# Performance work log

Hardware: AMD Instinct MI355X
Metric: run time of the kernel (lower is better)

The kernel has to match this reference:

```python
import jax, jax.numpy as jnp
import numpy as np
import math

D_MODEL = 1024
N_HEADS = 16
HEAD_DIM = D_MODEL // N_HEADS  # 64
SEQ_LEN = 4096
LINFORMER_K = 128
BATCH = 4


def setup_inputs() -> dict:
    key = jax.random.key(0)
    ks = jax.random.split(key, 8)
    s = 0.02  # small init so softmax is not saturated
    return {
        "x": jax.random.normal(ks[0], (BATCH, SEQ_LEN, D_MODEL), dtype=jnp.float32),
        "Wq": jax.random.normal(ks[1], (D_MODEL, D_MODEL), dtype=jnp.float32) * s,
        "bq": jnp.zeros((D_MODEL,), dtype=jnp.float32),
        "Wk": jax.random.normal(ks[2], (D_MODEL, D_MODEL), dtype=jnp.float32) * s,
        "bk": jnp.zeros((D_MODEL,), dtype=jnp.float32),
        "Wv": jax.random.normal(ks[3], (D_MODEL, D_MODEL), dtype=jnp.float32) * s,
        "bv": jnp.zeros((D_MODEL,), dtype=jnp.float32),
        "E": jax.random.normal(ks[4], (N_HEADS, LINFORMER_K, SEQ_LEN), dtype=jnp.float32) * s,
    }


def _split_heads(X):
    # [b, l, d_model] -> [b, h, l, head_dim]
    b, l, _ = X.shape
    return X.reshape(b, l, N_HEADS, HEAD_DIM).transpose(0, 2, 1, 3)


def reference(x, Wq, bq, Wk, bk, Wv, bv, E):
    # Projections (nn.Linear: x @ W.T + b)
    Q = _split_heads(x @ Wq.T + bq)  # [b, h, l, hd]
    K = _split_heads(x @ Wk.T + bk)
    V = _split_heads(x @ Wv.T + bv)
    b, h, l, d = Q.shape
    # l == SEQ_LEN so no padding needed (pad branch is a no-op here)
    # Low-rank projection of K/V along sequence: E [h, k, l]
    Kp = jnp.einsum('hkl,bhld->bhkd', E, K)  # [b, h, k, hd]
    Vp = jnp.einsum('hkl,bhld->bhkd', E, V)
    # Small-context attention
    dot = jnp.einsum('bhld,bhkd->bhlk', Q, Kp) / math.sqrt(HEAD_DIM)
    attn = jax.nn.softmax(dot, axis=-1)  # [b, h, l, k]
    Xo = jnp.einsum('bhlk,bhkd->bhld', attn, Vp)
    # combine heads: [b, h, l, hd] -> [b, l, d_model]
    out = Xo.transpose(0, 2, 1, 3).reshape(b, l, h * d)
    return out
```

## Files before the change

### kernel.cpp

```cpp
#include <hip/hip_runtime.h>

typedef __bf16 bf16x8 __attribute__((ext_vector_type(8)));
typedef float f32x4 __attribute__((ext_vector_type(4)));

#define AS1 __attribute__((address_space(1)))
#define AS3 __attribute__((address_space(3)))

__device__ __forceinline__ void gload_lds16(const void* g, void* l) {
    __builtin_amdgcn_global_load_lds((const AS1 void*)g, (AS3 void*)l, 16, 0, 0);
}

__device__ __forceinline__ unsigned short f2bf(float f) {
    unsigned u = __builtin_bit_cast(unsigned, f);
    u += 0x7fffu + ((u >> 16) & 1u);
    return (unsigned short)(u >> 16);
}

__device__ __forceinline__ float bf2f(unsigned short u) {
    return __builtin_bit_cast(float, (unsigned)u << 16);
}

__global__ __launch_bounds__(256) void cvt_kernel(const float* __restrict__ src,
                                                  unsigned short* __restrict__ dst, int n4) {
    int i = blockIdx.x * 256 + threadIdx.x;
    if (i >= n4) return;
    float4 v = reinterpret_cast<const float4*>(src)[i];
    ushort4 o;
    o.x = f2bf(v.x); o.y = f2bf(v.y); o.z = f2bf(v.z); o.w = f2bf(v.w);
    reinterpret_cast<ushort4*>(dst)[i] = o;
}

__global__ __launch_bounds__(256) void cvt_x_kernel(const float* __restrict__ x,
                                                    unsigned short* __restrict__ xb,
                                                    unsigned short* __restrict__ xT) {
    __shared__ unsigned short tile[64][68];
    const int t = threadIdx.x;
    const int b = blockIdx.z, l0 = blockIdx.y * 64, c0 = blockIdx.x * 64;
    const int r = t >> 4, c4 = t & 15;
#pragma unroll
    for (int p = 0; p < 4; p++) {
        int row = p * 16 + r;
        const float4 v = *(const float4*)&x[(size_t)(b * 4096 + l0 + row) * 1024 + c0 + c4 * 4];
        ushort4 o;
        o.x = f2bf(v.x); o.y = f2bf(v.y); o.z = f2bf(v.z); o.w = f2bf(v.w);
        *(ushort4*)&xb[(size_t)(b * 4096 + l0 + row) * 1024 + c0 + c4 * 4] = o;
        tile[c4 * 4 + 0][row] = o.x;
        tile[c4 * 4 + 1][row] = o.y;
        tile[c4 * 4 + 2][row] = o.z;
        tile[c4 * 4 + 3][row] = o.w;
    }
    __syncthreads();
#pragma unroll
    for (int p = 0; p < 4; p++) {
        int c = p * 16 + r;
        ushort4 o = *(const ushort4*)&tile[c][c4 * 4];
        *(ushort4*)&xT[(size_t)(b * 1024 + c0 + c) * 4096 + l0 + c4 * 4] = o;
    }
}

__global__ __launch_bounds__(256) void gemm_q(
        const unsigned short* __restrict__ xb, const unsigned short* __restrict__ Wb,
        const float* __restrict__ bq, unsigned short* __restrict__ Qb) {
    __shared__ unsigned short lA[2 * 128 * 32];
    __shared__ unsigned short lB[2 * 128 * 32];
    const int tid = threadIdx.x, w = tid >> 6, lane = tid & 63;
    const int m0 = blockIdx.y * 128, n0 = blockIdx.x * 128;
    const int srow = lane >> 2, scol = (lane & 3) * 8;
    const int l15 = lane & 15, quad = lane >> 4;
    const int wm = w >> 1, wn = w & 1;
    f32x4 acc[4][4] = {};
    for (int k0 = 0; k0 < 1024; k0 += 64) {
        __syncthreads();
#pragma unroll
        for (int s = 0; s < 2; s++) {
#pragma unroll
            for (int i = 0; i < 2; i++) {
                int t = w * 2 + i;
                gload_lds16(xb + (size_t)(m0 + t * 16 + srow) * 1024 + k0 + s * 32 + scol,
                            (char*)lA + (s * 8192 + t * 1024));
                gload_lds16(Wb + (size_t)(n0 + t * 16 + srow) * 1024 + k0 + s * 32 + scol,
                            (char*)lB + (s * 8192 + t * 1024));
            }
        }
        __syncthreads();
#pragma unroll
        for (int s = 0; s < 2; s++) {
            bf16x8 af[4], bfr[4];
#pragma unroll
            for (int mi = 0; mi < 4; mi++)
                af[mi] = *(const bf16x8*)&lA[(s * 128 + wm * 64 + mi * 16 + l15) * 32 + quad * 8];
#pragma unroll
            for (int ni = 0; ni < 4; ni++)
                bfr[ni] = *(const bf16x8*)&lB[(s * 128 + wn * 64 + ni * 16 + l15) * 32 + quad * 8];
#pragma unroll
            for (int mi = 0; mi < 4; mi++)
#pragma unroll
                for (int ni = 0; ni < 4; ni++)
                    acc[mi][ni] = __builtin_amdgcn_mfma_f32_16x16x32_bf16(af[mi], bfr[ni],
                                                                          acc[mi][ni], 0, 0, 0);
        }
    }
#pragma unroll
    for (int ni = 0; ni < 4; ni++) {
        int col = n0 + wn * 64 + ni * 16 + l15;
        float bias_v = bq[col];
#pragma unroll
        for (int mi = 0; mi < 4; mi++) {
            int row = m0 + wm * 64 + mi * 16 + quad * 4;
#pragma unroll
            for (int r = 0; r < 4; r++)
                Qb[(size_t)(row + r) * 1024 + col] = f2bf(acc[mi][ni][r] + bias_v);
        }
    }
}

__global__ __launch_bounds__(256) void gemm_ex(
        const unsigned short* __restrict__ Eb, const unsigned short* __restrict__ xTb,
        unsigned short* __restrict__ Exb) {
    __shared__ unsigned short lA[2 * 128 * 32];
    __shared__ unsigned short lB[2 * 128 * 32];
    const int tid = threadIdx.x, w = tid >> 6, lane = tid & 63;
    const int m0 = blockIdx.y * 128, n0 = blockIdx.x * 128;
    const unsigned short* xT = xTb + (size_t)blockIdx.z * 1024 * 4096;
    unsigned short* Ex = Exb + (size_t)blockIdx.z * 2048 * 1024;
    const int srow = lane >> 2, scol = (lane & 3) * 8;
    const int l15 = lane & 15, quad = lane >> 4;
    const int wm = w >> 1, wn = w & 1;
    f32x4 acc[4][4] = {};
    for (int k0 = 0; k0 < 4096; k0 += 64) {
        __syncthreads();
#pragma unroll
        for (int s = 0; s < 2; s++) {
#pragma unroll
            for (int i = 0; i < 2; i++) {
                int t = w * 2 + i;
                gload_lds16(Eb + (size_t)(m0 + t * 16 + srow) * 4096 + k0 + s * 32 + scol,
                            (char*)lA + (s * 8192 + t * 1024));
                gload_lds16(xT + (size_t)(n0 + t * 16 + srow) * 4096 + k0 + s * 32 + scol,
                            (char*)lB + (s * 8192 + t * 1024));
            }
        }
        __syncthreads();
#pragma unroll
        for (int s = 0; s < 2; s++) {
            bf16x8 af[4], bfr[4];
#pragma unroll
            for (int mi = 0; mi < 4; mi++)
                af[mi] = *(const bf16x8*)&lA[(s * 128 + wm * 64 + mi * 16 + l15) * 32 + quad * 8];
#pragma unroll
            for (int ni = 0; ni < 4; ni++)
                bfr[ni] = *(const bf16x8*)&lB[(s * 128 + wn * 64 + ni * 16 + l15) * 32 + quad * 8];
#pragma unroll
            for (int mi = 0; mi < 4; mi++)
#pragma unroll
                for (int ni = 0; ni < 4; ni++)
                    acc[mi][ni] = __builtin_amdgcn_mfma_f32_16x16x32_bf16(af[mi], bfr[ni],
                                                                          acc[mi][ni], 0, 0, 0);
        }
    }
#pragma unroll
    for (int ni = 0; ni < 4; ni++) {
        int col = n0 + wn * 64 + ni * 16 + l15;
#pragma unroll
        for (int mi = 0; mi < 4; mi++) {
            int row = m0 + wm * 64 + mi * 16 + quad * 4;
#pragma unroll
            for (int r = 0; r < 4; r++)
                Ex[(size_t)(row + r) * 1024 + col] = f2bf(acc[mi][ni][r]);
        }
    }
}

__global__ __launch_bounds__(256) void kpvp_small(
        const unsigned short* __restrict__ Exb, const unsigned short* __restrict__ Wb,
        const unsigned short* __restrict__ Eb, const float* __restrict__ bk,
        const float* __restrict__ bv,
        unsigned short* __restrict__ Kpb, unsigned short* __restrict__ VpTb) {
    __shared__ unsigned short Exsh[128 * 32];
    __shared__ unsigned short Wksh[64 * 32];
    __shared__ unsigned short Wvsh[64 * 32];
    __shared__ float EsumSh[128];
    const int tid = threadIdx.x, w = tid >> 6, lane = tid & 63;
    const int l15 = lane & 15, quad = lane >> 4;
    const int srow = lane >> 2, scol = (lane & 3) * 8;
    const int bh = blockIdx.x, b = bh >> 4, h = bh & 15;
    const unsigned short* Ex = Exb + ((size_t)b * 2048 + h * 128) * 1024;
    const unsigned short* Wk = Wb + 1048576 + (size_t)h * 64 * 1024;
    const unsigned short* Wv = Wb + 2097152 + (size_t)h * 64 * 1024;
    for (int r = w; r < 128; r += 4) {
        const unsigned short* er = Eb + ((size_t)h * 128 + r) * 4096;
        float s = 0.f;
#pragma unroll
        for (int i = 0; i < 8; i++) {
            ushort4 a = *(const ushort4*)&er[i * 512 + lane * 8];
            ushort4 b2 = *(const ushort4*)&er[i * 512 + lane * 8 + 4];
            s += bf2f(a.x) + bf2f(a.y) + bf2f(a.z) + bf2f(a.w);
            s += bf2f(b2.x) + bf2f(b2.y) + bf2f(b2.z) + bf2f(b2.w);
        }
#pragma unroll
        for (int off = 32; off >= 1; off >>= 1) s += __shfl_xor(s, off, 64);
        if (lane == 0) EsumSh[r] = s;
    }
    __syncthreads();
    f32x4 accK[2][4] = {};
    f32x4 accV[8] = {};
    for (int c0 = 0; c0 < 1024; c0 += 32) {
        __syncthreads();
#pragma unroll
        for (int i = 0; i < 2; i++) {
            int t = w * 2 + i;
            gload_lds16(Ex + (size_t)(t * 16 + srow) * 1024 + c0 + scol, (char*)Exsh + t * 1024);
        }
        gload_lds16(Wk + (size_t)(w * 16 + srow) * 1024 + c0 + scol, (char*)Wksh + w * 1024);
        gload_lds16(Wv + (size_t)(w * 16 + srow) * 1024 + c0 + scol, (char*)Wvsh + w * 1024);
        __syncthreads();
        bf16x8 aK[2], bK[4], aV, bV[8];
#pragma unroll
        for (int mi = 0; mi < 2; mi++)
            aK[mi] = *(const bf16x8*)&Exsh[((w * 2 + mi) * 16 + l15) * 32 + quad * 8];
#pragma unroll
        for (int nt = 0; nt < 4; nt++)
            bK[nt] = *(const bf16x8*)&Wksh[(nt * 16 + l15) * 32 + quad * 8];
        aV = *(const bf16x8*)&Wvsh[(w * 16 + l15) * 32 + quad * 8];
#pragma unroll
        for (int nt = 0; nt < 8; nt++)
            bV[nt] = *(const bf16x8*)&Exsh[(nt * 16 + l15) * 32 + quad * 8];
#pragma unroll
        for (int mi = 0; mi < 2; mi++)
#pragma unroll
            for (int nt = 0; nt < 4; nt++)
                accK[mi][nt] = __builtin_amdgcn_mfma_f32_16x16x32_bf16(aK[mi], bK[nt],
                                                                       accK[mi][nt], 0, 0, 0);
#pragma unroll
        for (int nt = 0; nt < 8; nt++)
            accV[nt] = __builtin_amdgcn_mfma_f32_16x16x32_bf16(aV, bV[nt], accV[nt], 0, 0, 0);
    }
    unsigned short* Kp = Kpb + (size_t)bh * 128 * 64;
    unsigned short* VpT = VpTb + (size_t)bh * 64 * 128;
#pragma unroll
    for (int mi = 0; mi < 2; mi++)
#pragma unroll
        for (int nt = 0; nt < 4; nt++) {
            int col = nt * 16 + l15;
            float bkv = bk[h * 64 + col];
#pragma unroll
            for (int r = 0; r < 4; r++) {
                int row = w * 32 + mi * 16 + quad * 4 + r;
                Kp[row * 64 + col] = f2bf(accK[mi][nt][r] + EsumSh[row] * bkv);
            }
        }
#pragma unroll
    for (int nt = 0; nt < 8; nt++) {
        int col = nt * 16 + l15;
        float es = EsumSh[col];
#pragma unroll
        for (int r = 0; r < 4; r++) {
            int row = w * 16 + quad * 4 + r;
            VpT[row * 128 + col] = f2bf(accV[nt][r] + es * bv[h * 64 + row]);
        }
    }
}

__global__ __launch_bounds__(256) void attn_kernel(
        const unsigned short* __restrict__ Qb, const unsigned short* __restrict__ Kpb,
        const unsigned short* __restrict__ VpTb, float* __restrict__ out) {
    __shared__ unsigned short P[4 * 16 * 136];
    const int tid = threadIdx.x, w = tid >> 6, lane = tid & 63;
    const int l15 = lane & 15, quad = lane >> 4;
    const int bh = blockIdx.y, b = bh >> 4, h = bh & 15;
    const int l0 = blockIdx.x * 64 + w * 16;
    const unsigned short* Qrow = Qb + (size_t)(b * 4096 + l0 + l15) * 1024 + h * 64;
    bf16x8 aq0 = *(const bf16x8*)&Qrow[quad * 8];
    bf16x8 aq1 = *(const bf16x8*)&Qrow[32 + quad * 8];
    const unsigned short* Kp = Kpb + (size_t)bh * 128 * 64;
    f32x4 acc[8];
#pragma unroll
    for (int kt = 0; kt < 8; kt++) {
        const unsigned short* kr = Kp + (size_t)(kt * 16 + l15) * 64;
        bf16x8 b0 = *(const bf16x8*)&kr[quad * 8];
        bf16x8 b1 = *(const bf16x8*)&kr[32 + quad * 8];
        f32x4 a = {};
        a = __builtin_amdgcn_mfma_f32_16x16x32_bf16(aq0, b0, a, 0, 0, 0);
        a = __builtin_amdgcn_mfma_f32_16x16x32_bf16(aq1, b1, a, 0, 0, 0);
        acc[kt] = a;
    }
    const float scale = 0.125f;
    float pr[8][4];
#pragma unroll
    for (int r = 0; r < 4; r++) {
        float m = -1e30f;
#pragma unroll
        for (int kt = 0; kt < 8; kt++) m = fmaxf(m, acc[kt][r]);
#pragma unroll
        for (int off = 8; off >= 1; off >>= 1) m = fmaxf(m, __shfl_xor(m, off, 64));
        float s = 0.f;
#pragma unroll
        for (int kt = 0; kt < 8; kt++) {
            float e = __expf(scale * (acc[kt][r] - m));
            pr[kt][r] = e;
            s += e;
        }
#pragma unroll
        for (int off = 8; off >= 1; off >>= 1) s += __shfl_xor(s, off, 64);
        float rinv = 1.0f / s;
#pragma unroll
        for (int kt = 0; kt < 8; kt++) pr[kt][r] *= rinv;
    }
    unsigned short* Pw = &P[w * 16 * 136];
#pragma unroll
    for (int kt = 0; kt < 8; kt++)
#pragma unroll
        for (int r = 0; r < 4; r++)
            Pw[(quad * 4 + r) * 136 + kt * 16 + l15] = f2bf(pr[kt][r]);
    __syncthreads();
    bf16x8 ap[4];
#pragma unroll
    for (int t = 0; t < 4; t++)
        ap[t] = *(const bf16x8*)&Pw[l15 * 136 + t * 32 + quad * 8];
    const unsigned short* Vp = VpTb + (size_t)bh * 64 * 128;
    f32x4 acco[4] = {};
#pragma unroll
    for (int nt = 0; nt < 4; nt++) {
        const unsigned short* vr = Vp + (size_t)(nt * 16 + l15) * 128;
#pragma unroll
        for (int t = 0; t < 4; t++) {
            bf16x8 bv = *(const bf16x8*)&vr[t * 32 + quad * 8];
            acco[nt] = __builtin_amdgcn_mfma_f32_16x16x32_bf16(ap[t], bv, acco[nt], 0, 0, 0);
        }
    }
#pragma unroll
    for (int nt = 0; nt < 4; nt++) {
        int col = h * 64 + nt * 16 + l15;
#pragma unroll
        for (int r = 0; r < 4; r++)
            out[(size_t)(b * 4096 + l0 + quad * 4 + r) * 1024 + col] = acco[nt][r];
    }
}

extern "C" void kernel_launch(void* const* d_in, const int* in_sizes, int n_in,
                              void* d_out, int out_size, void* d_ws, size_t ws_size,
                              hipStream_t stream) {
    const float* x  = (const float*)d_in[0];
    const float* Wq = (const float*)d_in[1];
    const float* bq = (const float*)d_in[2];
    const float* Wk = (const float*)d_in[3];
    const float* bk = (const float*)d_in[4];
    const float* Wv = (const float*)d_in[5];
    const float* bv = (const float*)d_in[6];
    const float* E  = (const float*)d_in[7];
    float* out = (float*)d_out;
    char* ws = (char*)d_ws;

    unsigned short* xb   = (unsigned short*)(ws);
    unsigned short* xTb  = (unsigned short*)(ws + 33554432);
    unsigned short* Wb   = (unsigned short*)(ws + 67108864);
    unsigned short* Qb   = (unsigned short*)(ws + 73400320);
    unsigned short* Eb   = (unsigned short*)(ws + 106954752);
    unsigned short* Exb  = (unsigned short*)(ws + 123731968);
    unsigned short* Kpb  = (unsigned short*)(ws + 140509184);
    unsigned short* VpTb = (unsigned short*)(ws + 141557760);
    if (ws_size < 142606336) return;

    cvt_x_kernel<<<dim3(16, 64, 4), 256, 0, stream>>>(x, xb, xTb);
    cvt_kernel<<<1024, 256, 0, stream>>>(Wq, Wb, 262144);
    cvt_kernel<<<1024, 256, 0, stream>>>(Wk, Wb + 1048576, 262144);
    cvt_kernel<<<1024, 256, 0, stream>>>(Wv, Wb + 2097152, 262144);
    cvt_kernel<<<8192, 256, 0, stream>>>(E, Eb, 2097152);
    gemm_q<<<dim3(8, 128), 256, 0, stream>>>(xb, Wb, bq, Qb);
    gemm_ex<<<dim3(8, 16, 4), 256, 0, stream>>>(Eb, xTb, Exb);
    kpvp_small<<<64, 256, 0, stream>>>(Exb, Wb, Eb, bk, bv, Kpb, VpTb);
    attn_kernel<<<dim3(64, 64), 256, 0, stream>>>(Qb, Kpb, VpTb, out);
}
```

Measured before the change: 416.4 us.

## Fuse conversion launches, merge Q and Ex GEMMs, split kpvp across more blocks

Combines the five conversion kernels into one launch and merges the Q-projection and E·x GEMMs into a single grid. The long-K Ex tiles are scheduled first so that the short Q tiles fill in behind them. The small K/V projection kernel goes from 64 blocks to 256 by splitting each head's 128 low-rank rows into four chunks, with double-buffered LDS staging. The aim is to cut launch overhead and raise occupancy in the under-parallelized kpvp stage. In exchange, each kpvp block reloads the full Wk/Wv slices, adding redundant memory traffic.

```diff
diff --git a/kernel.cpp b/kernel.cpp
--- a/kernel.cpp
+++ b/kernel.cpp
@@ -20,66 +20,95 @@
     return __builtin_bit_cast(float, (unsigned)u << 16);
 }
 
-__global__ __launch_bounds__(256) void cvt_kernel(const float* __restrict__ src,
-                                                  unsigned short* __restrict__ dst, int n4) {
-    int i = blockIdx.x * 256 + threadIdx.x;
-    if (i >= n4) return;
-    float4 v = reinterpret_cast<const float4*>(src)[i];
-    ushort4 o;
-    o.x = f2bf(v.x); o.y = f2bf(v.y); o.z = f2bf(v.z); o.w = f2bf(v.w);
-    reinterpret_cast<ushort4*>(dst)[i] = o;
-}
-
-__global__ __launch_bounds__(256) void cvt_x_kernel(const float* __restrict__ x,
-                                                    unsigned short* __restrict__ xb,
-                                                    unsigned short* __restrict__ xT) {
+__global__ __launch_bounds__(256) void fused_cvt(
+        const float* __restrict__ x, const float* __restrict__ Wq,
+        const float* __restrict__ Wk, const float* __restrict__ Wv,
+        const float* __restrict__ E,
+        unsigned short* __restrict__ xb, unsigned short* __restrict__ xT,
+        unsigned short* __restrict__ Wb, unsigned short* __restrict__ Eb) {
     __shared__ unsigned short tile[64][68];
-    const int t = threadIdx.x;
-    const int b = blockIdx.z, l0 = blockIdx.y * 64, c0 = blockIdx.x * 64;
-    const int r = t >> 4, c4 = t & 15;
-#pragma unroll
-    for (int p = 0; p < 4; p++) {
-        int row = p * 16 + r;
-        const float4 v = *(const float4*)&x[(size_t)(b * 4096 + l0 + row) * 1024 + c0 + c4 * 4];
+    const int id = blockIdx.x, t = threadIdx.x;
+    if (id < 4096) {
+        const int cx = id & 15, ly = (id >> 4) & 63, b = id >> 10;
+        const int l0 = ly * 64, c0 = cx * 64;
+        const int r = t >> 4, c4 = t & 15;
+#pragma unroll
+        for (int p = 0; p < 4; p++) {
+            int row = p * 16 + r;
+            const float4 v = *(const float4*)&x[(size_t)(b * 4096 + l0 + row) * 1024 + c0 + c4 * 4];
+            ushort4 o;
+            o.x = f2bf(v.x); o.y = f2bf(v.y); o.z = f2bf(v.z); o.w = f2bf(v.w);
+            *(ushort4*)&xb[(size_t)(b * 4096 + l0 + row) * 1024 + c0 + c4 * 4] = o;
+            tile[c4 * 4 + 0][row] = o.x;
+            tile[c4 * 4 + 1][row] = o.y;
+            tile[c4 * 4 + 2][row] = o.z;
+            tile[c4 * 4 + 3][row] = o.w;
+        }
+        __syncthreads();
+#pragma unroll
+        for (int p = 0; p < 4; p++) {
+            int c = p * 16 + r;
+            ushort4 o = *(const ushort4*)&tile[c][c4 * 4];
+            *(ushort4*)&xT[(size_t)(b * 1024 + c0 + c) * 4096 + l0 + c4 * 4] = o;
+        }
+    } else if (id < 7168) {
+        const int wi = id - 4096, which = wi >> 10;
+        const int i = (wi & 1023) * 256 + t;
+        const float* src = (which == 0) ? Wq : (which == 1 ? Wk : Wv);
+        float4 v = reinterpret_cast<const float4*>(src)[i];
         ushort4 o;
         o.x = f2bf(v.x); o.y = f2bf(v.y); o.z = f2bf(v.z); o.w = f2bf(v.w);
-        *(ushort4*)&xb[(size_t)(b * 4096 + l0 + row) * 1024 + c0 + c4 * 4] = o;
-        tile[c4 * 4 + 0][row] = o.x;
-        tile[c4 * 4 + 1][row] = o.y;
-        tile[c4 * 4 + 2][row] = o.z;
-        tile[c4 * 4 + 3][row] = o.w;
-    }
-    __syncthreads();
-#pragma unroll
-    for (int p = 0; p < 4; p++) {
-        int c = p * 16 + r;
-        ushort4 o = *(const ushort4*)&tile[c][c4 * 4];
-        *(ushort4*)&xT[(size_t)(b * 1024 + c0 + c) * 4096 + l0 + c4 * 4] = o;
-    }
-}
-
-__global__ __launch_bounds__(256) void gemm_q(
+        reinterpret_cast<ushort4*>(Wb + (size_t)which * 1048576)[i] = o;
+    } else {
+        const int i = (id - 7168) * 256 + t;
+        float4 v = reinterpret_cast<const float4*>(E)[i];
+        ushort4 o;
+        o.x = f2bf(v.x); o.y = f2bf(v.y); o.z = f2bf(v.z); o.w = f2bf(v.w);
+        reinterpret_cast<ushort4*>(Eb)[i] = o;
+    }
+}
+
+__global__ __launch_bounds__(256) void gemm_qex(
         const unsigned short* __restrict__ xb, const unsigned short* __restrict__ Wb,
-        const float* __restrict__ bq, unsigned short* __restrict__ Qb) {
+        const float* __restrict__ bq,
+        const unsigned short* __restrict__ Eb, const unsigned short* __restrict__ xTb,
+        unsigned short* __restrict__ Qb, unsigned short* __restrict__ Exb) {
     __shared__ unsigned short lA[2 * 128 * 32];
     __shared__ unsigned short lB[2 * 128 * 32];
     const int tid = threadIdx.x, w = tid >> 6, lane = tid & 63;
-    const int m0 = blockIdx.y * 128, n0 = blockIdx.x * 128;
     const int srow = lane >> 2, scol = (lane & 3) * 8;
     const int l15 = lane & 15, quad = lane >> 4;
     const int wm = w >> 1, wn = w & 1;
+    const int id = blockIdx.x;
+    const unsigned short *Aptr, *Bptr;
+    unsigned short* Cp;
+    int m0, n0, K;
+    size_t lda;
+    bool isQ;
+    if (id < 512) {
+        const int z = id >> 7, tt = id & 127;
+        n0 = (tt & 7) * 128; m0 = (tt >> 3) * 128;
+        Aptr = Eb; Bptr = xTb + (size_t)z * 1024 * 4096;
+        Cp = Exb + (size_t)z * 2048 * 1024;
+        K = 4096; lda = 4096; isQ = false;
+    } else {
+        const int tt = id - 512;
+        n0 = (tt & 7) * 128; m0 = (tt >> 3) * 128;
+        Aptr = xb; Bptr = Wb; Cp = Qb;
+        K = 1024; lda = 1024; isQ = true;
+    }
     f32x4 acc[4][4] = {};
-    for (int k0 = 0; k0 < 1024; k0 += 64) {
+    for (int k0 = 0; k0 < K; k0 += 64) {
         __syncthreads();
 #pragma unroll
         for (int s = 0; s < 2; s++) {
 #pragma unroll
             for (int i = 0; i < 2; i++) {
-                int t = w * 2 + i;
-                gload_lds16(xb + (size_t)(m0 + t * 16 + srow) * 1024 + k0 + s * 32 + scol,
-                            (char*)lA + (s * 8192 + t * 1024));
-                gload_lds16(Wb + (size_t)(n0 + t * 16 + srow) * 1024 + k0 + s * 32 + scol,
-                            (char*)lB + (s * 8192 + t * 1024));
+                int tt = w * 2 + i;
+                gload_lds16(Aptr + (size_t)(m0 + tt * 16 + srow) * lda + k0 + s * 32 + scol,
+                            (char*)lA + (s * 8192 + tt * 1024));
+                gload_lds16(Bptr + (size_t)(n0 + tt * 16 + srow) * lda + k0 + s * 32 + scol,
+                            (char*)lB + (s * 8192 + tt * 1024));
             }
         }
         __syncthreads();
@@ -103,92 +132,36 @@
 #pragma unroll
     for (int ni = 0; ni < 4; ni++) {
         int col = n0 + wn * 64 + ni * 16 + l15;
-        float bias_v = bq[col];
+        float bias_v = isQ ? bq[col] : 0.0f;
 #pragma unroll
         for (int mi = 0; mi < 4; mi++) {
             int row = m0 + wm * 64 + mi * 16 + quad * 4;
 #pragma unroll
             for (int r = 0; r < 4; r++)
-                Qb[(size_t)(row + r) * 1024 + col] = f2bf(acc[mi][ni][r] + bias_v);
-        }
-    }
-}
-
-__global__ __launch_bounds__(256) void gemm_ex(
-        const unsigned short* __restrict__ Eb, const unsigned short* __restrict__ xTb,
-        unsigned short* __restrict__ Exb) {
-    __shared__ unsigned short lA[2 * 128 * 32];
-    __shared__ unsigned short lB[2 * 128 * 32];
-    const int tid = threadIdx.x, w = tid >> 6, lane = tid & 63;
-    const int m0 = blockIdx.y * 128, n0 = blockIdx.x * 128;
-    const unsigned short* xT = xTb + (size_t)blockIdx.z * 1024 * 4096;
-    unsigned short* Ex = Exb + (size_t)blockIdx.z * 2048 * 1024;
-    const int srow = lane >> 2, scol = (lane & 3) * 8;
-    const int l15 = lane & 15, quad = lane >> 4;
-    const int wm = w >> 1, wn = w & 1;
-    f32x4 acc[4][4] = {};
-    for (int k0 = 0; k0 < 4096; k0 += 64) {
-        __syncthreads();
-#pragma unroll
-        for (int s = 0; s < 2; s++) {
-#pragma unroll
-            for (int i = 0; i < 2; i++) {
-                int t = w * 2 + i;
-                gload_lds16(Eb + (size_t)(m0 + t * 16 + srow) * 4096 + k0 + s * 32 + scol,
-                            (char*)lA + (s * 8192 + t * 1024));
-                gload_lds16(xT + (size_t)(n0 + t * 16 + srow) * 4096 + k0 + s * 32 + scol,
-                            (char*)lB + (s * 8192 + t * 1024));
-            }
-        }
-        __syncthreads();
-#pragma unroll
-        for (int s = 0; s < 2; s++) {
-            bf16x8 af[4], bfr[4];
-#pragma unroll
-            for (int mi = 0; mi < 4; mi++)
-                af[mi] = *(const bf16x8*)&lA[(s * 128 + wm * 64 + mi * 16 + l15) * 32 + quad * 8];
-#pragma unroll
-            for (int ni = 0; ni < 4; ni++)
-                bfr[ni] = *(const bf16x8*)&lB[(s * 128 + wn * 64 + ni * 16 + l15) * 32 + quad * 8];
-#pragma unroll
-            for (int mi = 0; mi < 4; mi++)
-#pragma unroll
-                for (int ni = 0; ni < 4; ni++)
-                    acc[mi][ni] = __builtin_amdgcn_mfma_f32_16x16x32_bf16(af[mi], bfr[ni],
-                                                                          acc[mi][ni], 0, 0, 0);
-        }
-    }
-#pragma unroll
-    for (int ni = 0; ni < 4; ni++) {
-        int col = n0 + wn * 64 + ni * 16 + l15;
-#pragma unroll
-        for (int mi = 0; mi < 4; mi++) {
-            int row = m0 + wm * 64 + mi * 16 + quad * 4;
-#pragma unroll
-            for (int r = 0; r < 4; r++)
-                Ex[(size_t)(row + r) * 1024 + col] = f2bf(acc[mi][ni][r]);
-        }
-    }
-}
-
-__global__ __launch_bounds__(256) void kpvp_small(
+                Cp[(size_t)(row + r) * 1024 + col] = f2bf(acc[mi][ni][r] + bias_v);
+        }
+    }
+}
+
+__global__ __launch_bounds__(256) void kpvp4(
         const unsigned short* __restrict__ Exb, const unsigned short* __restrict__ Wb,
         const unsigned short* __restrict__ Eb, const float* __restrict__ bk,
         const float* __restrict__ bv,
         unsigned short* __restrict__ Kpb, unsigned short* __restrict__ VpTb) {
-    __shared__ unsigned short Exsh[128 * 32];
-    __shared__ unsigned short Wksh[64 * 32];
-    __shared__ unsigned short Wvsh[64 * 32];
-    __shared__ float EsumSh[128];
+    __shared__ unsigned short Exsh[2 * 32 * 32];
+    __shared__ unsigned short Wksh[2 * 64 * 32];
+    __shared__ unsigned short Wvsh[2 * 64 * 32];
+    __shared__ float EsumSh[32];
     const int tid = threadIdx.x, w = tid >> 6, lane = tid & 63;
     const int l15 = lane & 15, quad = lane >> 4;
     const int srow = lane >> 2, scol = (lane & 3) * 8;
-    const int bh = blockIdx.x, b = bh >> 4, h = bh & 15;
-    const unsigned short* Ex = Exb + ((size_t)b * 2048 + h * 128) * 1024;
+    const int bh = blockIdx.x & 63, q = blockIdx.x >> 6;
+    const int b = bh >> 4, h = bh & 15;
+    const unsigned short* Ex = Exb + ((size_t)b * 2048 + h * 128 + q * 32) * 1024;
     const unsigned short* Wk = Wb + 1048576 + (size_t)h * 64 * 1024;
     const unsigned short* Wv = Wb + 2097152 + (size_t)h * 64 * 1024;
-    for (int r = w; r < 128; r += 4) {
-        const unsigned short* er = Eb + ((size_t)h * 128 + r) * 4096;
+    for (int r = w; r < 32; r += 4) {
+        const unsigned short* er = Eb + ((size_t)(h * 128 + q * 32 + r)) * 4096;
         float s = 0.f;
 #pragma unroll
         for (int i = 0; i < 8; i++) {
@@ -201,63 +174,76 @@
         for (int off = 32; off >= 1; off >>= 1) s += __shfl_xor(s, off, 64);
         if (lane == 0) EsumSh[r] = s;
     }
+    f32x4 accK[4] = {};
+    f32x4 accV[2][2] = {};
+    auto STAGE = [&](int t, int s) {
+        const int c0 = t * 32;
+        if (w < 2)
+            gload_lds16(Ex + (size_t)(w * 16 + srow) * 1024 + c0 + scol,
+                        (char*)Exsh + s * 2048 + w * 1024);
+        gload_lds16(Wk + (size_t)(w * 16 + srow) * 1024 + c0 + scol,
+                    (char*)Wksh + s * 4096 + w * 1024);
+        gload_lds16(Wv + (size_t)(w * 16 + srow) * 1024 + c0 + scol,
+                    (char*)Wvsh + s * 4096 + w * 1024);
+    };
+    auto COMPUTE = [&](int s) {
+        if (w < 2) {
+            bf16x8 af = *(const bf16x8*)&Exsh[s * 1024 + (w * 16 + l15) * 32 + quad * 8];
+#pragma unroll
+            for (int nt = 0; nt < 4; nt++) {
+                bf16x8 bb = *(const bf16x8*)&Wksh[s * 2048 + (nt * 16 + l15) * 32 + quad * 8];
+                accK[nt] = __builtin_amdgcn_mfma_f32_16x16x32_bf16(af, bb, accK[nt], 0, 0, 0);
+            }
+        } else {
+            bf16x8 av[2], be[2];
+#pragma unroll
+            for (int mi = 0; mi < 2; mi++)
+                av[mi] = *(const bf16x8*)&Wvsh[s * 2048 + (((w - 2) * 2 + mi) * 16 + l15) * 32 + quad * 8];
+#pragma unroll
+            for (int n = 0; n < 2; n++)
+                be[n] = *(const bf16x8*)&Exsh[s * 1024 + (n * 16 + l15) * 32 + quad * 8];
+#pragma unroll
+            for (int mi = 0; mi < 2; mi++)
+#pragma unroll
+                for (int n = 0; n < 2; n++)
+                    accV[mi][n] = __builtin_amdgcn_mfma_f32_16x16x32_bf16(av[mi], be[n],
+                                                                          accV[mi][n], 0, 0, 0);
+        }
+    };
+    STAGE(0, 0);
     __syncthreads();
-    f32x4 accK[2][4] = {};
-    f32x4 accV[8] = {};
-    for (int c0 = 0; c0 < 1024; c0 += 32) {
+    for (int t = 0; t < 31; ++t) {
+        STAGE(t + 1, (t + 1) & 1);
+        COMPUTE(t & 1);
         __syncthreads();
-#pragma unroll
-        for (int i = 0; i < 2; i++) {
-            int t = w * 2 + i;
-            gload_lds16(Ex + (size_t)(t * 16 + srow) * 1024 + c0 + scol, (char*)Exsh + t * 1024);
-        }
-        gload_lds16(Wk + (size_t)(w * 16 + srow) * 1024 + c0 + scol, (char*)Wksh + w * 1024);
-        gload_lds16(Wv + (size_t)(w * 16 + srow) * 1024 + c0 + scol, (char*)Wvsh + w * 1024);
-        __syncthreads();
-        bf16x8 aK[2], bK[4], aV, bV[8];
-#pragma unroll
-        for (int mi = 0; mi < 2; mi++)
-            aK[mi] = *(const bf16x8*)&Exsh[((w * 2 + mi) * 16 + l15) * 32 + quad * 8];
-#pragma unroll
-        for (int nt = 0; nt < 4; nt++)
-            bK[nt] = *(const bf16x8*)&Wksh[(nt * 16 + l15) * 32 + quad * 8];
-        aV = *(const bf16x8*)&Wvsh[(w * 16 + l15) * 32 + quad * 8];
-#pragma unroll
-        for (int nt = 0; nt < 8; nt++)
-            bV[nt] = *(const bf16x8*)&Exsh[(nt * 16 + l15) * 32 + quad * 8];
-#pragma unroll
-        for (int mi = 0; mi < 2; mi++)
-#pragma unroll
-            for (int nt = 0; nt < 4; nt++)
-                accK[mi][nt] = __builtin_amdgcn_mfma_f32_16x16x32_bf16(aK[mi], bK[nt],
-                                                                       accK[mi][nt], 0, 0, 0);
-#pragma unroll
-        for (int nt = 0; nt < 8; nt++)
-            accV[nt] = __builtin_amdgcn_mfma_f32_16x16x32_bf16(aV, bV[nt], accV[nt], 0, 0, 0);
-    }
+    }
+    COMPUTE(1);
     unsigned short* Kp = Kpb + (size_t)bh * 128 * 64;
     unsigned short* VpT = VpTb + (size_t)bh * 64 * 128;
-#pragma unroll
-    for (int mi = 0; mi < 2; mi++)
+    if (w < 2) {
 #pragma unroll
         for (int nt = 0; nt < 4; nt++) {
             int col = nt * 16 + l15;
             float bkv = bk[h * 64 + col];
 #pragma unroll
             for (int r = 0; r < 4; r++) {
-                int row = w * 32 + mi * 16 + quad * 4 + r;
-                Kp[row * 64 + col] = f2bf(accK[mi][nt][r] + EsumSh[row] * bkv);
+                int krow = w * 16 + quad * 4 + r;
+                Kp[(q * 32 + krow) * 64 + col] = f2bf(accK[nt][r] + EsumSh[krow] * bkv);
             }
         }
-#pragma unroll
-    for (int nt = 0; nt < 8; nt++) {
-        int col = nt * 16 + l15;
-        float es = EsumSh[col];
-#pragma unroll
-        for (int r = 0; r < 4; r++) {
-            int row = w * 16 + quad * 4 + r;
-            VpT[row * 128 + col] = f2bf(accV[nt][r] + es * bv[h * 64 + row]);
-        }
+    } else {
+#pragma unroll
+        for (int mi = 0; mi < 2; mi++)
+#pragma unroll
+            for (int n = 0; n < 2; n++) {
+                int kcol = n * 16 + l15;
+                float es = EsumSh[kcol];
+#pragma unroll
+                for (int r = 0; r < 4; r++) {
+                    int d = ((w - 2) * 2 + mi) * 16 + quad * 4 + r;
+                    VpT[d * 128 + q * 32 + kcol] = f2bf(accV[mi][n][r] + es * bv[h * 64 + d]);
+                }
+            }
     }
 }
 
@@ -361,13 +347,8 @@
     unsigned short* VpTb = (unsigned short*)(ws + 141557760);
     if (ws_size < 142606336) return;
 
-    cvt_x_kernel<<<dim3(16, 64, 4), 256, 0, stream>>>(x, xb, xTb);
-    cvt_kernel<<<1024, 256, 0, stream>>>(Wq, Wb, 262144);
-    cvt_kernel<<<1024, 256, 0, stream>>>(Wk, Wb + 1048576, 262144);
-    cvt_kernel<<<1024, 256, 0, stream>>>(Wv, Wb + 2097152, 262144);
-    cvt_kernel<<<8192, 256, 0, stream>>>(E, Eb, 2097152);
-    gemm_q<<<dim3(8, 128), 256, 0, stream>>>(xb, Wb, bq, Qb);
-    gemm_ex<<<dim3(8, 16, 4), 256, 0, stream>>>(Eb, xTb, Exb);
-    kpvp_small<<<64, 256, 0, stream>>>(Exb, Wb, Eb, bk, bv, Kpb, VpTb);
+    fused_cvt<<<15360, 256, 0, stream>>>(x, Wq, Wk, Wv, E, xb, xTb, Wb, Eb);
+    gemm_qex<<<1536, 256, 0, stream>>>(xb, Wb, bq, Eb, xTb, Qb, Exb);
+    kpvp4<<<256, 256, 0, stream>>>(Exb, Wb, Eb, bk, bv, Kpb, VpTb);
     attn_kernel<<<dim3(64, 64), 256, 0, stream>>>(Qb, Kpb, VpTb, out);
 }
```

Measured after the change: 381.1 us. -8.5%, faster.
